# Kernel tuning notes

Hardware: AMD Instinct MI355X
Metric: run time of the kernel (lower is better)

## Reference

```python
import jax, jax.numpy as jnp
import numpy as np

N_NODES = 40000
N_EDGES = 640000
D = 128
L = 3
EPS_NORM = 1e-12  # F.normalize eps


def setup_inputs() -> dict:
    key = jax.random.key(0)
    ks = jax.random.split(key, 12)
    s = 1.0 / np.sqrt(D)  # keep activations in a sane range
    x = jax.random.normal(ks[0], (N_NODES, D), dtype=jnp.float32)
    edge_index = jax.random.randint(ks[1], (2, N_EDGES), 0, N_NODES, dtype=jnp.int64)
    return {
        "x": x,
        "edge_index": edge_index,
        "Wk": jax.random.normal(ks[2], (L, D, D), dtype=jnp.float32) * s,
        "bk": jax.random.normal(ks[3], (L, D), dtype=jnp.float32) * s,
        "Wq": jax.random.normal(ks[4], (L, D, D), dtype=jnp.float32) * s,
        "bq": jax.random.normal(ks[5], (L, D), dtype=jnp.float32) * s,
        "Wv": jax.random.normal(ks[6], (L, D, D), dtype=jnp.float32) * s,
        "bv": jax.random.normal(ks[7], (L, D), dtype=jnp.float32) * s,
        "Ws": jax.random.normal(ks[8], (L, D, D), dtype=jnp.float32) * s,
        "gamma": jnp.ones((L, D), dtype=jnp.float32),
        "beta": jnp.zeros((L, D), dtype=jnp.float32),
    }


def _l2norm(h, axis):
    n = jnp.sqrt(jnp.sum(h * h, axis=axis, keepdims=True))
    return h / jnp.maximum(n, EPS_NORM)


def reference(x, edge_index, Wk, bk, Wq, bq, Wv, bv, Ws, gamma, beta):
    src = edge_index[0]  # message source j
    dst = edge_index[1]  # message target i
    n = x.shape[0]
    h = x
    for l in range(Wk.shape[0]):  # fixed small num_layers
        x_in = h
        # ResGatedGraphConv: out_i = W_skip x_i + sum_j sigmoid(k_i + q_j) * v_j
        k = x_in @ Wk[l].T + bk[l]
        q = x_in @ Wq[l].T + bq[l]
        v = x_in @ Wv[l].T + bv[l]
        msg = jax.nn.sigmoid(k[dst] + q[src]) * v[src]          # [E, D]
        agg = jax.ops.segment_sum(msg, dst, num_segments=n)     # [N, D]
        out = agg + x_in @ Ws[l].T                              # no conv bias (has_batch_norm)
        # BatchNorm1d in eval mode with running_mean=0, running_var=1
        out = out * gamma[l] + beta[l]
        out = jax.nn.relu(out)
        out = _l2norm(out, axis=1)        # per-layer has_l2_norm
        h = x_in + out                    # skipsum
    return _l2norm(h, axis=-1)            # final_l2_norm
```

## Files before the change

kernel.cpp:

```cpp
#include <hip/hip_runtime.h>
#include <math.h>

#define NN 40000
#define NE 640000
#define DD 128
#define NL 3
#define SCAN_NBLK ((NN + 255) / 256)
#define NEG_LOG2E -1.4426950408889634f

typedef short s16x8 __attribute__((ext_vector_type(8)));
typedef float f32x4 __attribute__((ext_vector_type(4)));
typedef float f32x2 __attribute__((ext_vector_type(2)));
typedef unsigned short ushort_t;

__device__ __forceinline__ ushort_t f2bf(float f) {
    unsigned int u = __float_as_uint(f);
    u = (u + 0x7FFFu + ((u >> 16) & 1u)) >> 16;
    return (ushort_t)u;
}
__device__ __forceinline__ float bf2f(ushort_t h) {
    return __uint_as_float(((unsigned int)h) << 16);
}

__global__ void convert_hist_kernel(const int* __restrict__ ei,
                                    int* __restrict__ srcs, int* __restrict__ dsts,
                                    int* __restrict__ count) {
    __shared__ int sh_is64;
    if (threadIdx.x == 0) {
        int is64 = 1;
        for (int k = 0; k < 32; ++k)
            if (ei[2 * k + 1] != 0) { is64 = 0; break; }
        sh_is64 = is64;
    }
    __syncthreads();
    int e = blockIdx.x * blockDim.x + threadIdx.x;
    if (e >= NE) return;
    int s, d;
    if (sh_is64) {
        s = ei[2 * e];
        d = ei[2 * (NE + e)];
    } else {
        s = ei[e];
        d = ei[NE + e];
    }
    srcs[e] = s;
    dsts[e] = d;
    atomicAdd(&count[d], 1);
}

__global__ __launch_bounds__(256) void scan1_kernel(const int* __restrict__ count,
                                                    int* __restrict__ row_ptr,
                                                    int* __restrict__ blocksum) {
    __shared__ int tmp[256];
    int t = threadIdx.x;
    int i = blockIdx.x * 256 + t;
    int v = (i < NN) ? count[i] : 0;
    tmp[t] = v;
    __syncthreads();
    for (int off = 1; off < 256; off <<= 1) {
        int u = (t >= off) ? tmp[t - off] : 0;
        __syncthreads();
        tmp[t] += u;
        __syncthreads();
    }
    if (i < NN) row_ptr[i] = tmp[t] - v;
    if (t == 255) blocksum[blockIdx.x] = tmp[255];
}

__global__ __launch_bounds__(256) void scan2_kernel(const int* __restrict__ blocksum,
                                                    int* __restrict__ blockoff) {
    __shared__ int tmp[256];
    int t = threadIdx.x;
    int v = (t < SCAN_NBLK) ? blocksum[t] : 0;
    tmp[t] = v;
    __syncthreads();
    for (int off = 1; off < 256; off <<= 1) {
        int u = (t >= off) ? tmp[t - off] : 0;
        __syncthreads();
        tmp[t] += u;
        __syncthreads();
    }
    if (t < SCAN_NBLK) blockoff[t] = tmp[t] - v;
}

__global__ void scan3_kernel(int* __restrict__ row_ptr, const int* __restrict__ blockoff,
                             int* __restrict__ cursor) {
    int i = blockIdx.x * blockDim.x + threadIdx.x;
    if (i >= NN) return;
    int r = row_ptr[i] + blockoff[i >> 8];
    row_ptr[i] = r;
    cursor[i] = r;
    if (i == 0) row_ptr[NN] = NE;
}

__global__ void scatter_kernel(const int* __restrict__ srcs, const int* __restrict__ dsts,
                               int* __restrict__ cursor, int* __restrict__ csr_src) {
    int e = blockIdx.x * blockDim.x + threadIdx.x;
    if (e >= NE) return;
    int i = dsts[e];
    int pos = atomicAdd(&cursor[i], 1);
    csr_src[pos] = srcs[e] << 9;
}

__global__ void cvt_x_kernel(const float* __restrict__ x, ushort_t* __restrict__ xb) {
    int i = blockIdx.x * blockDim.x + threadIdx.x;
    if (i >= NN * DD / 8) return;
    const float* p = x + (size_t)i * 8;
    s16x8 o;
#pragma unroll
    for (int j = 0; j < 8; ++j) o[j] = (short)f2bf(p[j]);
    *(s16x8*)&xb[(size_t)i * 8] = o;
}

__global__ void cvt_w_kernel(const float* __restrict__ Wk, const float* __restrict__ Wq,
                             const float* __restrict__ Wv, const float* __restrict__ Ws,
                             ushort_t* __restrict__ wall) {
    int g = blockIdx.x * blockDim.x + threadIdx.x;
    if (g >= NL * 4 * DD * DD / 8) return;
    size_t flat = (size_t)g * 8;
    int l = (int)(flat / (4 * DD * DD));
    int r = (int)(flat % (4 * DD * DD));
    int m = r / (DD * DD);
    int o = r % (DD * DD);
    const float* src;
    switch (m) {
        case 0: src = Wk; break;
        case 1: src = Wq; break;
        case 2: src = Wv; break;
        default: src = Ws; break;
    }
    const float* p = src + (size_t)l * DD * DD + o;
    s16x8 ov;
#pragma unroll
    for (int j = 0; j < 8; ++j) ov[j] = (short)f2bf(p[j]);
    *(s16x8*)&wall[flat] = ov;
}

__global__ __launch_bounds__(256) void gemm4_mfma(
    const ushort_t* __restrict__ xb,
    const ushort_t* __restrict__ wall,
    const float* __restrict__ bk, const float* __restrict__ bq,
    const float* __restrict__ bv,
    ushort_t* __restrict__ ks, ushort_t* __restrict__ gat,
    int layer) {
    __shared__ ushort_t wlds[DD * DD];

    const int t = threadIdx.x;
    const int w = t >> 6;
    const int lane = t & 63;
    const int row0 = blockIdx.x * 64;

    const int arow = row0 + w * 16 + (lane & 15);
    const ushort_t* ap = xb + (size_t)arow * DD + ((lane >> 4) << 3);
    s16x8 afrag[4];
#pragma unroll
    for (int kb = 0; kb < 4; ++kb) afrag[kb] = *(const s16x8*)(ap + kb * 32);

    const int dlow = lane & 15;
    const int dbase = dlow * 256;
    const int swz = (lane & 7) << 4;
    const int g16 = (lane >> 4) << 4;

    unsigned int qs[8][2];

    for (int m = 0; m < 4; ++m) {
        if (m) __syncthreads();
        const ushort_t* wsrc = wall + (((size_t)layer * 4 + m) << 14);
#pragma unroll
        for (int p = 0; p < 8; ++p) {
            int g = p * 256 + t;
            int d = g >> 4;
            int s = g & 15;
            int byteoff = d * 256 + ((s * 16) ^ ((d & 7) << 4));
            *(s16x8*)((char*)wlds + byteoff) = *(const s16x8*)(wsrc + (size_t)g * 8);
        }
        __syncthreads();

        f32x4 acc[8];
#pragma unroll
        for (int ct = 0; ct < 8; ++ct) acc[ct] = (f32x4){0.f, 0.f, 0.f, 0.f};

#pragma unroll
        for (int kb = 0; kb < 4; ++kb) {
#pragma unroll
            for (int ct = 0; ct < 8; ++ct) {
                s16x8 bfrag = *(const s16x8*)((char*)wlds + ct * 4096 + dbase +
                                              ((kb * 64 + g16) ^ swz));
                acc[ct] = __builtin_amdgcn_mfma_f32_16x16x32_bf16(afrag[kb], bfrag,
                                                                  acc[ct], 0, 0, 0);
            }
        }

        const int rbase = row0 + w * 16 + ((lane >> 4) << 2);
#pragma unroll
        for (int ct = 0; ct < 8; ++ct) {
            int c0 = ct * 16 + dlow;
            if (m == 0) {
                float bval = bk[layer * DD + c0];
#pragma unroll
                for (int j = 0; j < 4; ++j)
                    __builtin_nontemporal_store(
                        f2bf((acc[ct][j] + bval) * NEG_LOG2E),
                        &ks[(size_t)(rbase + j) * 256 + c0]);
            } else if (m == 1) {
                float bval = bq[layer * DD + c0];
                qs[ct][0] = (unsigned int)f2bf((acc[ct][0] + bval) * NEG_LOG2E) |
                            ((unsigned int)f2bf((acc[ct][1] + bval) * NEG_LOG2E) << 16);
                qs[ct][1] = (unsigned int)f2bf((acc[ct][2] + bval) * NEG_LOG2E) |
                            ((unsigned int)f2bf((acc[ct][3] + bval) * NEG_LOG2E) << 16);
            } else if (m == 2) {
                float bval = bv[layer * DD + c0];
#pragma unroll
                for (int j = 0; j < 4; ++j) {
                    unsigned int q16 = (qs[ct][j >> 1] >> ((j & 1) * 16)) & 0xFFFFu;
                    unsigned int val = q16 | ((unsigned int)f2bf(acc[ct][j] + bval) << 16);
                    *(unsigned int*)&gat[(size_t)(rbase + j) * 256 + 2 * c0] = val;
                }
            } else {
#pragma unroll
                for (int j = 0; j < 4; ++j)
                    __builtin_nontemporal_store(
                        f2bf(acc[ct][j]),
                        &ks[(size_t)(rbase + j) * 256 + 128 + c0]);
            }
        }
    }
}

__global__ __launch_bounds__(256) void agg_kernel(
    const ushort_t* __restrict__ ks,
    const ushort_t* __restrict__ gat,
    const int* __restrict__ row_ptr,
    const int* __restrict__ csr_src,
    const float* __restrict__ gamma, const float* __restrict__ beta,
    ushort_t* __restrict__ xb,
    float* __restrict__ out_f32,
    int layer, int final_norm) {
    int wid = __builtin_amdgcn_readfirstlane(
        (int)((blockIdx.x * blockDim.x + threadIdx.x) >> 6));
    if (wid >= NN) return;
    int lane = threadIdx.x & 63;
    int d0 = lane * 2;

    const ushort_t* ksp = ks + ((unsigned)wid << 8);
    unsigned kword = __builtin_nontemporal_load((const unsigned*)&ksp[d0]);
    unsigned sword = __builtin_nontemporal_load((const unsigned*)&ksp[128 + d0]);
    float kx = __uint_as_float(kword << 16);
    float ky = __uint_as_float(kword & 0xFFFF0000u);
    float ax = __uint_as_float(sword << 16);
    float ay = __uint_as_float(sword & 0xFFFF0000u);

    const char* gbase = (const char*)gat;
    const unsigned qvoff = 8u * (unsigned)lane;
    int s = row_ptr[wid];
    int e = row_ptr[wid + 1];
    int idx = s;

#define GATE(wrd, KK, AA)                                                     \
    do {                                                                      \
        float qf = __uint_as_float((wrd) << 16);                              \
        float vf = __uint_as_float((wrd) & 0xFFFF0000u);                      \
        float g = __builtin_amdgcn_rcpf(1.0f +                                \
                    __builtin_amdgcn_exp2f(KK + qf));                         \
        AA = fmaf(g, vf, AA);                                                 \
    } while (0)

    while (idx + 8 <= e) {
        uint2 wv[8];
#pragma unroll
        for (int u = 0; u < 8; ++u) {
            unsigned b = (unsigned)csr_src[idx + u];
            wv[u] = *(const uint2*)(gbase + b + qvoff);
        }
#pragma unroll
        for (int u = 0; u < 8; ++u) {
            GATE(wv[u].x, kx, ax);
            GATE(wv[u].y, ky, ay);
        }
        idx += 8;
    }
    while (idx + 2 <= e) {
        unsigned b0 = (unsigned)csr_src[idx];
        unsigned b1 = (unsigned)csr_src[idx + 1];
        uint2 w0 = *(const uint2*)(gbase + b0 + qvoff);
        uint2 w1 = *(const uint2*)(gbase + b1 + qvoff);
        GATE(w0.x, kx, ax);
        GATE(w0.y, ky, ay);
        GATE(w1.x, kx, ax);
        GATE(w1.y, ky, ay);
        idx += 2;
    }
    if (idx < e) {
        unsigned b0 = (unsigned)csr_src[idx];
        uint2 w0 = *(const uint2*)(gbase + b0 + qvoff);
        GATE(w0.x, kx, ax);
        GATE(w0.y, ky, ay);
    }
#undef GATE

    float gx = gamma[layer * DD + d0], gy = gamma[layer * DD + d0 + 1];
    float btx = beta[layer * DD + d0], bty = beta[layer * DD + d0 + 1];
    float rx = fmaxf(ax * gx + btx, 0.f);
    float ry = fmaxf(ay * gy + bty, 0.f);

    float ss = rx * rx + ry * ry;
#pragma unroll
    for (int m = 1; m < 64; m <<= 1) ss += __shfl_xor(ss, m);
    float inv = __builtin_amdgcn_rcpf(fmaxf(sqrtf(ss), 1e-12f));

    unsigned xw = *(const unsigned*)&xb[((unsigned)wid << 7) + d0];
    float hx = __uint_as_float(xw << 16) + rx * inv;
    float hy = __uint_as_float(xw & 0xFFFF0000u) + ry * inv;

    if (final_norm) {
        float s2 = hx * hx + hy * hy;
#pragma unroll
        for (int m = 1; m < 64; m <<= 1) s2 += __shfl_xor(s2, m);
        float inv2 = __builtin_amdgcn_rcpf(fmaxf(sqrtf(s2), 1e-12f));
        f32x2 o;
        o.x = hx * inv2;
        o.y = hy * inv2;
        __builtin_nontemporal_store(o, (f32x2*)&out_f32[(size_t)wid * DD + d0]);
    } else {
        unsigned ob = (unsigned)f2bf(hx) | ((unsigned)f2bf(hy) << 16);
        *(unsigned*)&xb[((unsigned)wid << 7) + d0] = ob;
    }
}

extern "C" void kernel_launch(void* const* d_in, const int* in_sizes, int n_in,
                              void* d_out, int out_size, void* d_ws, size_t ws_size,
                              hipStream_t stream) {
    const float* x     = (const float*)d_in[0];
    const int*   ei    = (const int*)d_in[1];
    const float* Wk    = (const float*)d_in[2];
    const float* bk    = (const float*)d_in[3];
    const float* Wq    = (const float*)d_in[4];
    const float* bq    = (const float*)d_in[5];
    const float* Wv    = (const float*)d_in[6];
    const float* bv    = (const float*)d_in[7];
    const float* Ws    = (const float*)d_in[8];
    const float* gamma = (const float*)d_in[9];
    const float* beta  = (const float*)d_in[10];
    float* out = (float*)d_out;

    ushort_t* ks  = (ushort_t*)d_ws;
    ushort_t* gat = ks + (size_t)NN * 256;
    ushort_t* xb  = gat + (size_t)NN * 256;
    ushort_t* wall = xb + (size_t)NN * DD;
    int* srcs     = (int*)(wall + (size_t)NL * 4 * DD * DD);
    int* dsts     = srcs + NE;
    int* count    = dsts + NE;
    int* cursor   = count + NN;
    int* row_ptr  = cursor + NN;
    int* csr_src  = row_ptr + (NN + 1);
    int* blocksum = csr_src + NE;
    int* blockoff = blocksum + SCAN_NBLK;

    (void)hipMemsetAsync(count, 0, NN * sizeof(int), stream);
    convert_hist_kernel<<<(NE + 255) / 256, 256, 0, stream>>>(ei, srcs, dsts, count);
    scan1_kernel<<<SCAN_NBLK, 256, 0, stream>>>(count, row_ptr, blocksum);
    scan2_kernel<<<1, 256, 0, stream>>>(blocksum, blockoff);
    scan3_kernel<<<(NN + 255) / 256, 256, 0, stream>>>(row_ptr, blockoff, cursor);
    scatter_kernel<<<(NE + 255) / 256, 256, 0, stream>>>(srcs, dsts, cursor, csr_src);

    cvt_x_kernel<<<(NN * DD / 8 + 255) / 256, 256, 0, stream>>>(x, xb);
    cvt_w_kernel<<<(NL * 4 * DD * DD / 8 + 255) / 256, 256, 0, stream>>>(Wk, Wq, Wv, Ws, wall);

    for (int l = 0; l < NL; ++l) {
        gemm4_mfma<<<NN / 64, 256, 0, stream>>>(xb, wall, bk, bq, bv, ks, gat, l);
        agg_kernel<<<(NN * 64) / 256, 256, 0, stream>>>(
            ks, gat, row_ptr, csr_src, gamma, beta, xb,
            (l == NL - 1) ? out : nullptr, l, (l == NL - 1) ? 1 : 0);
    }
}
```

Before: 282.0 us.

## Fuse weight conversion into edge prep, read fp32 x directly in layer 0

Merges the weight bf16 conversion into the edge-index conversion/histogram kernel as extra blocks, and removes the standalone x-to-bf16 conversion kernel. Layer 0's GEMM now converts fp32 x to bf16 on the fly, and layer 0's aggregation reads the fp32 residual directly. The aggregation gather loop is also widened from 8 to 16 edges per iteration, with 4-wide and scalar tails. These changes cut two kernel launches and an extra pass over x, at the cost of more registers in the gather loop.

Measured after the change: 281.7 us. Within noise of the previous version (-0.1%).

```diff
diff --git a/kernel.cpp b/kernel.cpp
--- a/kernel.cpp
+++ b/kernel.cpp
@@ -6,6 +6,8 @@
 #define DD 128
 #define NL 3
 #define SCAN_NBLK ((NN + 255) / 256)
+#define NB_CONV ((NE + 255) / 256)
+#define NB_W    (NL * 4 * DD * DD / 8 / 256)
 #define NEG_LOG2E -1.4426950408889634f
 
 typedef short s16x8 __attribute__((ext_vector_type(8)));
@@ -22,30 +24,55 @@
     return __uint_as_float(((unsigned int)h) << 16);
 }
 
-__global__ void convert_hist_kernel(const int* __restrict__ ei,
-                                    int* __restrict__ srcs, int* __restrict__ dsts,
-                                    int* __restrict__ count) {
-    __shared__ int sh_is64;
-    if (threadIdx.x == 0) {
-        int is64 = 1;
-        for (int k = 0; k < 32; ++k)
-            if (ei[2 * k + 1] != 0) { is64 = 0; break; }
-        sh_is64 = is64;
-    }
-    __syncthreads();
-    int e = blockIdx.x * blockDim.x + threadIdx.x;
-    if (e >= NE) return;
-    int s, d;
-    if (sh_is64) {
-        s = ei[2 * e];
-        d = ei[2 * (NE + e)];
+__global__ void pre_kernel(const int* __restrict__ ei,
+                           int* __restrict__ srcs, int* __restrict__ dsts,
+                           int* __restrict__ count,
+                           const float* __restrict__ Wk, const float* __restrict__ Wq,
+                           const float* __restrict__ Wv, const float* __restrict__ Ws,
+                           ushort_t* __restrict__ wall) {
+    int bid = blockIdx.x;
+    if (bid < NB_CONV) {
+        __shared__ int sh_is64;
+        if (threadIdx.x == 0) {
+            int is64 = 1;
+            for (int k = 0; k < 32; ++k)
+                if (ei[2 * k + 1] != 0) { is64 = 0; break; }
+            sh_is64 = is64;
+        }
+        __syncthreads();
+        int e = bid * 256 + threadIdx.x;
+        if (e >= NE) return;
+        int s, d;
+        if (sh_is64) {
+            s = ei[2 * e];
+            d = ei[2 * (NE + e)];
+        } else {
+            s = ei[e];
+            d = ei[NE + e];
+        }
+        srcs[e] = s;
+        dsts[e] = d;
+        atomicAdd(&count[d], 1);
     } else {
-        s = ei[e];
-        d = ei[NE + e];
-    }
-    srcs[e] = s;
-    dsts[e] = d;
-    atomicAdd(&count[d], 1);
+        int g = (bid - NB_CONV) * 256 + threadIdx.x;
+        size_t flat = (size_t)g * 8;
+        int l = (int)(flat / (4 * DD * DD));
+        int r = (int)(flat % (4 * DD * DD));
+        int m = r / (DD * DD);
+        int o = r % (DD * DD);
+        const float* src;
+        switch (m) {
+            case 0: src = Wk; break;
+            case 1: src = Wq; break;
+            case 2: src = Wv; break;
+            default: src = Ws; break;
+        }
+        const float* p = src + (size_t)l * DD * DD + o;
+        s16x8 ov;
+#pragma unroll
+        for (int j = 0; j < 8; ++j) ov[j] = (short)f2bf(p[j]);
+        *(s16x8*)&wall[flat] = ov;
+    }
 }
 
 __global__ __launch_bounds__(256) void scan1_kernel(const int* __restrict__ count,
@@ -102,42 +129,9 @@
     csr_src[pos] = srcs[e] << 9;
 }
 
-__global__ void cvt_x_kernel(const float* __restrict__ x, ushort_t* __restrict__ xb) {
-    int i = blockIdx.x * blockDim.x + threadIdx.x;
-    if (i >= NN * DD / 8) return;
-    const float* p = x + (size_t)i * 8;
-    s16x8 o;
-#pragma unroll
-    for (int j = 0; j < 8; ++j) o[j] = (short)f2bf(p[j]);
-    *(s16x8*)&xb[(size_t)i * 8] = o;
-}
-
-__global__ void cvt_w_kernel(const float* __restrict__ Wk, const float* __restrict__ Wq,
-                             const float* __restrict__ Wv, const float* __restrict__ Ws,
-                             ushort_t* __restrict__ wall) {
-    int g = blockIdx.x * blockDim.x + threadIdx.x;
-    if (g >= NL * 4 * DD * DD / 8) return;
-    size_t flat = (size_t)g * 8;
-    int l = (int)(flat / (4 * DD * DD));
-    int r = (int)(flat % (4 * DD * DD));
-    int m = r / (DD * DD);
-    int o = r % (DD * DD);
-    const float* src;
-    switch (m) {
-        case 0: src = Wk; break;
-        case 1: src = Wq; break;
-        case 2: src = Wv; break;
-        default: src = Ws; break;
-    }
-    const float* p = src + (size_t)l * DD * DD + o;
-    s16x8 ov;
-#pragma unroll
-    for (int j = 0; j < 8; ++j) ov[j] = (short)f2bf(p[j]);
-    *(s16x8*)&wall[flat] = ov;
-}
-
 __global__ __launch_bounds__(256) void gemm4_mfma(
     const ushort_t* __restrict__ xb,
+    const float* __restrict__ xf,
     const ushort_t* __restrict__ wall,
     const float* __restrict__ bk, const float* __restrict__ bq,
     const float* __restrict__ bv,
@@ -151,10 +145,24 @@
     const int row0 = blockIdx.x * 64;
 
     const int arow = row0 + w * 16 + (lane & 15);
-    const ushort_t* ap = xb + (size_t)arow * DD + ((lane >> 4) << 3);
     s16x8 afrag[4];
-#pragma unroll
-    for (int kb = 0; kb < 4; ++kb) afrag[kb] = *(const s16x8*)(ap + kb * 32);
+    if (xf) {
+        const float* apf = xf + (size_t)arow * DD + ((lane >> 4) << 3);
+#pragma unroll
+        for (int kb = 0; kb < 4; ++kb) {
+            f32x4 lo = *(const f32x4*)(apf + kb * 32);
+            f32x4 hi = *(const f32x4*)(apf + kb * 32 + 4);
+#pragma unroll
+            for (int j = 0; j < 4; ++j) {
+                afrag[kb][j] = (short)f2bf(lo[j]);
+                afrag[kb][j + 4] = (short)f2bf(hi[j]);
+            }
+        }
+    } else {
+        const ushort_t* ap = xb + (size_t)arow * DD + ((lane >> 4) << 3);
+#pragma unroll
+        for (int kb = 0; kb < 4; ++kb) afrag[kb] = *(const s16x8*)(ap + kb * 32);
+    }
 
     const int dlow = lane & 15;
     const int dbase = dlow * 256;
@@ -233,6 +241,7 @@
     const int* __restrict__ row_ptr,
     const int* __restrict__ csr_src,
     const float* __restrict__ gamma, const float* __restrict__ beta,
+    const float* __restrict__ hin_f32,
     ushort_t* __restrict__ xb,
     float* __restrict__ out_f32,
     int layer, int final_norm) {
@@ -265,36 +274,40 @@
         AA = fmaf(g, vf, AA);                                                 \
     } while (0)
 
-    while (idx + 8 <= e) {
-        uint2 wv[8];
-#pragma unroll
-        for (int u = 0; u < 8; ++u) {
+    while (idx + 16 <= e) {
+        uint2 wv[16];
+#pragma unroll
+        for (int u = 0; u < 16; ++u) {
             unsigned b = (unsigned)csr_src[idx + u];
             wv[u] = *(const uint2*)(gbase + b + qvoff);
         }
 #pragma unroll
-        for (int u = 0; u < 8; ++u) {
+        for (int u = 0; u < 16; ++u) {
             GATE(wv[u].x, kx, ax);
             GATE(wv[u].y, ky, ay);
         }
-        idx += 8;
-    }
-    while (idx + 2 <= e) {
-        unsigned b0 = (unsigned)csr_src[idx];
-        unsigned b1 = (unsigned)csr_src[idx + 1];
-        uint2 w0 = *(const uint2*)(gbase + b0 + qvoff);
-        uint2 w1 = *(const uint2*)(gbase + b1 + qvoff);
-        GATE(w0.x, kx, ax);
-        GATE(w0.y, ky, ay);
-        GATE(w1.x, kx, ax);
-        GATE(w1.y, ky, ay);
-        idx += 2;
-    }
-    if (idx < e) {
+        idx += 16;
+    }
+    while (idx + 4 <= e) {
+        uint2 wv[4];
+#pragma unroll
+        for (int u = 0; u < 4; ++u) {
+            unsigned b = (unsigned)csr_src[idx + u];
+            wv[u] = *(const uint2*)(gbase + b + qvoff);
+        }
+#pragma unroll
+        for (int u = 0; u < 4; ++u) {
+            GATE(wv[u].x, kx, ax);
+            GATE(wv[u].y, ky, ay);
+        }
+        idx += 4;
+    }
+    while (idx < e) {
         unsigned b0 = (unsigned)csr_src[idx];
         uint2 w0 = *(const uint2*)(gbase + b0 + qvoff);
         GATE(w0.x, kx, ax);
         GATE(w0.y, ky, ay);
+        ++idx;
     }
 #undef GATE
 
@@ -308,9 +321,16 @@
     for (int m = 1; m < 64; m <<= 1) ss += __shfl_xor(ss, m);
     float inv = __builtin_amdgcn_rcpf(fmaxf(sqrtf(ss), 1e-12f));
 
-    unsigned xw = *(const unsigned*)&xb[((unsigned)wid << 7) + d0];
-    float hx = __uint_as_float(xw << 16) + rx * inv;
-    float hy = __uint_as_float(xw & 0xFFFF0000u) + ry * inv;
+    float hx, hy;
+    if (hin_f32) {
+        f32x2 xi = *(const f32x2*)&hin_f32[(size_t)wid * DD + d0];
+        hx = xi.x + rx * inv;
+        hy = xi.y + ry * inv;
+    } else {
+        unsigned xw = *(const unsigned*)&xb[((unsigned)wid << 7) + d0];
+        hx = __uint_as_float(xw << 16) + rx * inv;
+        hy = __uint_as_float(xw & 0xFFFF0000u) + ry * inv;
+    }
 
     if (final_norm) {
         float s2 = hx * hx + hy * hy;
@@ -357,19 +377,19 @@
     int* blockoff = blocksum + SCAN_NBLK;
 
     (void)hipMemsetAsync(count, 0, NN * sizeof(int), stream);
-    convert_hist_kernel<<<(NE + 255) / 256, 256, 0, stream>>>(ei, srcs, dsts, count);
+    pre_kernel<<<NB_CONV + NB_W, 256, 0, stream>>>(ei, srcs, dsts, count,
+                                                   Wk, Wq, Wv, Ws, wall);
     scan1_kernel<<<SCAN_NBLK, 256, 0, stream>>>(count, row_ptr, blocksum);
     scan2_kernel<<<1, 256, 0, stream>>>(blocksum, blockoff);
     scan3_kernel<<<(NN + 255) / 256, 256, 0, stream>>>(row_ptr, blockoff, cursor);
     scatter_kernel<<<(NE + 255) / 256, 256, 0, stream>>>(srcs, dsts, cursor, csr_src);
 
-    cvt_x_kernel<<<(NN * DD / 8 + 255) / 256, 256, 0, stream>>>(x, xb);
-    cvt_w_kernel<<<(NL * 4 * DD * DD / 8 + 255) / 256, 256, 0, stream>>>(Wk, Wq, Wv, Ws, wall);
-
     for (int l = 0; l < NL; ++l) {
-        gemm4_mfma<<<NN / 64, 256, 0, stream>>>(xb, wall, bk, bq, bv, ks, gat, l);
+        gemm4_mfma<<<NN / 64, 256, 0, stream>>>(xb, (l == 0) ? x : nullptr, wall,
+                                                bk, bq, bv, ks, gat, l);
         agg_kernel<<<(NN * 64) / 256, 256, 0, stream>>>(
-            ks, gat, row_ptr, csr_src, gamma, beta, xb,
+            ks, gat, row_ptr, csr_src, gamma, beta,
+            (l == 0) ? x : nullptr, xb,
             (l == NL - 1) ? out : nullptr, l, (l == NL - 1) ? 1 : 0);
     }
 }
```
